# Performance work log

Measured on AMD Instinct MI355X. Metric: run time of the kernel, lower is better.

Reference implementation:

```python
import jax, jax.numpy as jnp
import numpy as np
import math

NHEADS = 8


def pos_encoding_2d(d_model, H, W):
    dm = d_model // 2
    div = jnp.exp(jnp.arange(0, dm, 2, dtype=jnp.float32) * (-math.log(10000.0) / dm))  # [dm//2]
    pw = jnp.arange(W, dtype=jnp.float32)[:, None] * div  # [W, dm//2]
    ph = jnp.arange(H, dtype=jnp.float32)[:, None] * div  # [H, dm//2]
    pe = jnp.zeros((d_model, H, W), jnp.float32)
    pe = pe.at[0:dm:2].set(jnp.broadcast_to(jnp.sin(pw).T[:, None, :], (dm // 2, H, W)))
    pe = pe.at[1:dm:2].set(jnp.broadcast_to(jnp.cos(pw).T[:, None, :], (dm // 2, H, W)))
    pe = pe.at[dm::2].set(jnp.broadcast_to(jnp.sin(ph).T[:, :, None], (dm // 2, H, W)))
    pe = pe.at[dm + 1::2].set(jnp.broadcast_to(jnp.cos(ph).T[:, :, None], (dm // 2, H, W)))
    return pe


def conv_same(x, w, b):
    y = jax.lax.conv_general_dilated(x, w, (1, 1), 'SAME',
                                     dimension_numbers=('NCHW', 'OIHW', 'NCHW'))
    return y + b[None, :, None, None]


def layernorm(x, g, b, eps=1e-5):
    mu = x.mean(-1, keepdims=True)
    var = ((x - mu) ** 2).mean(-1, keepdims=True)
    return (x - mu) / jnp.sqrt(var + eps) * g + b


def setup_inputs() -> dict:
    key = jax.random.key(0)
    B, C, H, W = 8, 256, 32, 32
    KQV, NH, K = 64, NHEADS, 3
    ks = jax.random.split(key, 16)
    s_conv = 1.0 / math.sqrt(C * K * K)
    s_lin = 1.0 / math.sqrt(NH * KQV)
    s_ff = 1.0 / math.sqrt(C)
    return {
        'x': jax.random.normal(ks[0], (B, C, H, W), jnp.float32),
        'Wk': jax.random.normal(ks[1], (NH * KQV, C, K, K), jnp.float32) * s_conv,
        'bk': jax.random.normal(ks[2], (NH * KQV,), jnp.float32) * s_conv,
        'Wq': jax.random.normal(ks[3], (NH * KQV, C, K, K), jnp.float32) * s_conv,
        'bq': jax.random.normal(ks[4], (NH * KQV,), jnp.float32) * s_conv,
        'Wv': jax.random.normal(ks[5], (NH * KQV, C, K, K), jnp.float32) * s_conv,
        'bv': jax.random.normal(ks[6], (NH * KQV,), jnp.float32) * s_conv,
        'Wproj': jax.random.normal(ks[7], (C, NH * KQV), jnp.float32) * s_lin,
        'bproj': jax.random.normal(ks[8], (C,), jnp.float32) * s_lin,
        'ln_g': jnp.ones((C,), jnp.float32),
        'ln_b': jnp.zeros((C,), jnp.float32),
        'W1': jax.random.normal(ks[9], (C, C), jnp.float32) * s_ff,
        'b1': jax.random.normal(ks[10], (C,), jnp.float32) * s_ff,
        'W2': jax.random.normal(ks[11], (C, C), jnp.float32) * s_ff,
        'b2': jax.random.normal(ks[12], (C,), jnp.float32) * s_ff,
    }


def reference(x, Wk, bk, Wq, bq, Wv, bv, Wproj, bproj, ln_g, ln_b, W1, b1, W2, b2):
    B, C, H, W = x.shape
    N = H * W
    pe = pos_encoding_2d(C, H, W)
    xp = x + pe[None]                                   # [B,C,H,W]
    xflat = xp.reshape(B, C, N).transpose(0, 2, 1)      # [B,N,C]

    def heads(w, b):
        return conv_same(xp, w, b).reshape(B, NHEADS, -1, N)  # [B,h,c,N]

    k = heads(Wk, bk)
    q = heads(Wq, bq)
    v = heads(Wv, bv)
    scores = jnp.einsum('bhcn,bhcm->bhnm', k, q) / N    # K^T Q / N, [B,h,N,N]
    sm = jax.nn.softmax(scores, axis=1)                 # Softmax2d -> over HEAD dim (faithful)
    att = jnp.einsum('bhnm,bhcm->bhnc', sm, v)          # [B,h,N,c]
    att = att.transpose(0, 2, 3, 1).reshape(B, N, -1)   # [B,N,c*h] (channel-major, head-minor)
    attproj = att @ Wproj.T + bproj                     # [B,N,C]
    addnormed = layernorm(xflat + attproj, ln_g, ln_b)
    h1 = addnormed @ W1.T + b1
    h1 = jnp.where(h1 > 0, h1, 0.1 * h1)                # LeakyReLU(0.1)
    h2 = h1 @ W2.T + b2
    out = layernorm(h2 + addnormed, ln_g, ln_b)         # same LN params reused (faithful)
    return out.transpose(0, 2, 1).reshape(B, C, H, W)
```

## Files before the change

### kernel.cpp

```cpp
#include <hip/hip_runtime.h>
#include <stdint.h>

typedef __attribute__((ext_vector_type(8))) short short8;
typedef __attribute__((ext_vector_type(4))) short s16x4;
typedef __attribute__((ext_vector_type(4))) float f32x4;

#define DEVI __device__ __forceinline__

#if __has_builtin(__builtin_amdgcn_mfma_f32_16x16x16_bf16)
#define MFMA16(a, b, c) __builtin_amdgcn_mfma_f32_16x16x16_bf16(a, b, c, 0, 0, 0)
#else
#define MFMA16(a, b, c) __builtin_amdgcn_mfma_f32_16x16x16bf16_1k(a, b, c, 0, 0, 0)
#endif

DEVI unsigned short f2bf(float f) {
  union { float f; uint32_t u; } v; v.f = f;
  return (unsigned short)((v.u + 0x7fffu + ((v.u >> 16) & 1u)) >> 16);
}

DEVI float bf2f(uint32_t hi16) {
  union { uint32_t u; float f; } v; v.u = hi16;
  return v.f;
}

DEVI uint32_t pkbf(float a, float b) {
  union { float f; uint32_t u; } x, y; x.f = a; y.f = b;
  return ((x.u + 0x8000u) >> 16) | (((y.u + 0x8000u) >> 16) << 16);
}

DEVI void gload_lds16(const void* g, void* l) {
  __builtin_amdgcn_global_load_lds(
      (const __attribute__((address_space(1))) uint32_t*)g,
      (__attribute__((address_space(3))) uint32_t*)l, 16, 0, 0);
}

__global__ void k_petab(float* __restrict__ T, float* __restrict__ zp) {
  int c = threadIdx.x;
  zp[c] = 0.0f;
  int idx = ((c >= 128) ? c - 128 : c) >> 1;
  float freq = expf(-(float)idx * (logf(10000.0f) / 64.0f));
  for (int p = 0; p < 32; ++p) {
    float ang = (float)p * freq;
    T[c * 32 + p] = (c & 1) ? cosf(ang) : sinf(ang);
  }
}

__global__ __launch_bounds__(256) void k_xpt(const float* __restrict__ x,
                                             const float* __restrict__ T,
                                             unsigned short* __restrict__ xpt_bf,
                                             float* __restrict__ xpt_f) {
  __shared__ __align__(16) float tile[32][36];
  const int b = blockIdx.z, c0 = blockIdx.x * 32, n0 = blockIdx.y * 32;
  const int t = threadIdx.x;
  {
    const int cl = t >> 3, ng = (t & 7) * 4;
    const int c = c0 + cl;
    float4 v = *(const float4*)(x + ((size_t)b * 256 + c) * 1024 + n0 + ng);
    float p0, p1, p2, p3;
    if (c < 128) {
      p0 = T[c * 32 + ng + 0]; p1 = T[c * 32 + ng + 1];
      p2 = T[c * 32 + ng + 2]; p3 = T[c * 32 + ng + 3];
    } else {
      p0 = p1 = p2 = p3 = T[c * 32 + (n0 >> 5)];
    }
    tile[ng + 0][cl] = v.x + p0;
    tile[ng + 1][cl] = v.y + p1;
    tile[ng + 2][cl] = v.z + p2;
    tile[ng + 3][cl] = v.w + p3;
  }
  __syncthreads();
  {
    const int nl = t >> 3, cg = (t & 7) * 4;
    float o0 = tile[nl][cg + 0], o1 = tile[nl][cg + 1];
    float o2 = tile[nl][cg + 2], o3 = tile[nl][cg + 3];
    size_t row = (size_t)b * 1024 + n0 + nl;
    *(float4*)(xpt_f + row * 256 + c0 + cg) = make_float4(o0, o1, o2, o3);
    uint32_t lo = (uint32_t)f2bf(o0) | ((uint32_t)f2bf(o1) << 16);
    uint32_t hi = (uint32_t)f2bf(o2) | ((uint32_t)f2bf(o3) << 16);
    *(uint2*)(xpt_bf + row * 256 + c0 + cg) = make_uint2(lo, hi);
  }
}

__global__ void k_packall(const float* __restrict__ Wk, const float* __restrict__ Wq,
                          const float* __restrict__ Wv, const float* __restrict__ bk,
                          const float* __restrict__ bq, const float* __restrict__ bv,
                          const float* __restrict__ Wproj, const float* __restrict__ W1,
                          const float* __restrict__ W2, unsigned short* __restrict__ Wpack,
                          float* __restrict__ bias_kqv, unsigned short* __restrict__ WprojP,
                          unsigned short* __restrict__ W1b, unsigned short* __restrict__ W2b) {
  int bid = blockIdx.x;
  if (bid < 13824) {
    int i = bid * 256 + threadIdx.x;
    if (i >= 1536 * 2304) return;
    int o = i / 2304, kn = i % 2304;
    int ci = kn & 255, khw = kn >> 8;
    const float* src = (o < 512) ? Wk : ((o < 1024) ? Wq : Wv);
    int oo = o & 511;
    Wpack[i] = f2bf(src[((size_t)oo * 256 + ci) * 9 + khw]);
  } else {
    int i = (bid - 13824) * 256 + threadIdx.x;
    if (i < 1536)
      bias_kqv[i] = (i < 512) ? bk[i] : ((i < 1024) ? bq[i - 512] : bv[i - 1024]);
    {
      int j = i >> 9, f = i & 511;
      int h = f >> 6, c = f & 63;
      unsigned short v = f2bf(Wproj[(size_t)j * 512 + c * 8 + h]);
      WprojP[(size_t)j * 1024 + f] = v;
      WprojP[(size_t)j * 1024 + 512 + f] = v;
    }
    if (i < 65536) {
      W1b[i] = f2bf(W1[i]);
      W2b[i] = f2bf(W2[i]);
    }
  }
}

__global__ __launch_bounds__(256, 2) void k_gemm_conv(const unsigned short* __restrict__ xpt,
                                                      const unsigned short* __restrict__ Wp,
                                                      unsigned short* __restrict__ kqv,
                                                      const float* __restrict__ bias,
                                                      const char* __restrict__ zp) {
  __shared__ __align__(16) unsigned short As[2][128 * 64];
  __shared__ __align__(16) unsigned short Bs[2][128 * 64];
  const int tid = threadIdx.x, l = tid & 63, w = tid >> 6;
  const int wm = w >> 1, wn = w & 1, g = l >> 4, ln = l & 15;
  const int m0 = blockIdx.x * 128, n0 = blockIdx.y * 128;
  const int swz = (l & 7) ^ (l >> 3);

  int rA[4];
  const char* pAbase[4];
  const char* pA[4];
#pragma unroll
  for (int j = 0; j < 4; ++j) {
    int r = m0 + (w * 4 + j) * 8 + (l >> 3);
    rA[j] = r;
    pAbase[j] = (const char*)xpt + ((size_t)r * 256 + swz * 8) * 2;
  }
  const char* pB[4];
#pragma unroll
  for (int j = 0; j < 4; ++j) {
    int r = n0 + (w * 4 + j) * 8 + (l >> 3);
    pB[j] = (const char*)Wp + ((size_t)r * 2304 + swz * 8) * 2;
  }

  f32x4 acc[4][4] = {};

  auto setA = [&](int khw) {
    int d3 = (khw * 11) >> 5;
    int dy = d3 - 1, dx = khw - d3 * 3 - 1;
    int off = (dy * 32 + dx) * 512;
#pragma unroll
    for (int j = 0; j < 4; ++j) {
      int y = ((rA[j] >> 5) & 31) + dy;
      int x = (rA[j] & 31) + dx;
      pA[j] = (((unsigned)y < 32u) && ((unsigned)x < 32u)) ? (pAbase[j] + off) : zp;
    }
  };
  auto STAGE = [&](int buf) {
#pragma unroll
    for (int j = 0; j < 4; ++j) {
      gload_lds16(pA[j], (char*)As + buf * 16384 + (w * 4 + j) * 1024);
      pA[j] += 128;
    }
#pragma unroll
    for (int j = 0; j < 4; ++j) {
      gload_lds16(pB[j], (char*)Bs + buf * 16384 + (w * 4 + j) * 1024);
      pB[j] += 128;
    }
  };
  auto COMPUTE = [&](int buf) {
    const char* Ab2 = (const char*)As + buf * 16384;
    const char* Bb2 = (const char*)Bs + buf * 16384;
#pragma unroll
    for (int kk = 0; kk < 2; ++kk) {
      short8 af[4], bfr[4];
#pragma unroll
      for (int fm = 0; fm < 4; ++fm)
        af[fm] = *(const short8*)(Ab2 + (wm * 64 + fm * 16 + ln) * 128 +
                                  (((kk * 4 + g) ^ (ln & 7)) * 16));
#pragma unroll
      for (int fn = 0; fn < 4; ++fn)
        bfr[fn] = *(const short8*)(Bb2 + (wn * 64 + fn * 16 + ln) * 128 +
                                   (((kk * 4 + g) ^ (ln & 7)) * 16));
#pragma unroll
      for (int fm = 0; fm < 4; ++fm)
#pragma unroll
        for (int fn = 0; fn < 4; ++fn)
          acc[fm][fn] = __builtin_amdgcn_mfma_f32_16x16x32_bf16(af[fm], bfr[fn], acc[fm][fn], 0, 0, 0);
    }
  };

  setA(0);
  STAGE(0);
#pragma unroll
  for (int s = 0; s < 36; ++s) {
    const int buf = s & 1;
    if (s < 35) {
      if (((s + 1) & 3) == 0) setA((s + 1) >> 2);
      STAGE(buf ^ 1);
      asm volatile("s_waitcnt vmcnt(8)" ::: "memory");
    } else {
      asm volatile("s_waitcnt vmcnt(0)" ::: "memory");
    }
    __builtin_amdgcn_s_barrier();
    __builtin_amdgcn_sched_barrier(0);
    COMPUTE(buf);
    asm volatile("s_waitcnt lgkmcnt(0)" ::: "memory");
    __builtin_amdgcn_s_barrier();
    __builtin_amdgcn_sched_barrier(0);
  }

#pragma unroll
  for (int fm = 0; fm < 4; ++fm)
#pragma unroll
    for (int fn = 0; fn < 4; ++fn) {
      int col = n0 + wn * 64 + fn * 16 + ln;
      float bb = bias[col];
#pragma unroll
      for (int r = 0; r < 4; ++r) {
        int row = m0 + wm * 64 + fm * 16 + g * 4 + r;
        kqv[(size_t)row * 1536 + col] = f2bf(acc[fm][fn][r] + bb);
      }
    }
}

template <int EPI, bool ASPLIT>
__global__ __launch_bounds__(256) void k_gemm64(const unsigned short* __restrict__ A,
                                                const unsigned short* __restrict__ B,
                                                void* __restrict__ Cout,
                                                const float* __restrict__ bias,
                                                const float* __restrict__ resid,
                                                int N, int K) {
  __shared__ __align__(16) unsigned short As[128 * 64];
  __shared__ __align__(16) unsigned short Bs[64 * 64];
  const int tid = threadIdx.x, l = tid & 63, w = tid >> 6;
  const int g = l >> 4, ln = l & 15;
  const int m0 = blockIdx.x * 128, n0 = blockIdx.y * 64;
  const int swz = (l & 7) ^ (l >> 3);
  f32x4 acc[2][4] = {};

  for (int kt = 0; kt < K; kt += 64) {
#pragma unroll
    for (int j = 0; j < 4; ++j) {
      int seg = w * 4 + j;
      int r8 = seg * 8 + (l >> 3);
      const char* src;
      if (ASPLIT)
        src = (const char*)A + (((size_t)(kt >> 9) * 8192 * 512) +
                                (size_t)(m0 + r8) * 512 + (kt & 511) + swz * 8) * 2;
      else
        src = (const char*)A + ((size_t)(m0 + r8) * K + kt + swz * 8) * 2;
      gload_lds16(src, (char*)As + seg * 1024);
    }
#pragma unroll
    for (int j = 0; j < 2; ++j) {
      int seg = w * 2 + j;
      int r8 = seg * 8 + (l >> 3);
      gload_lds16((const char*)B + ((size_t)(n0 + r8) * K + kt + swz * 8) * 2,
                  (char*)Bs + seg * 1024);
    }
    __syncthreads();
#pragma unroll
    for (int kk = 0; kk < 2; ++kk) {
      short8 af[2], bfr[4];
#pragma unroll
      for (int fm = 0; fm < 2; ++fm)
        af[fm] = *(const short8*)((const char*)As + (w * 32 + fm * 16 + ln) * 128 +
                                  (((kk * 4 + g) ^ (ln & 7)) * 16));
#pragma unroll
      for (int fn = 0; fn < 4; ++fn)
        bfr[fn] = *(const short8*)((const char*)Bs + (fn * 16 + ln) * 128 +
                                   (((kk * 4 + g) ^ (ln & 7)) * 16));
#pragma unroll
      for (int fm = 0; fm < 2; ++fm)
#pragma unroll
        for (int fn = 0; fn < 4; ++fn)
          acc[fm][fn] = __builtin_amdgcn_mfma_f32_16x16x32_bf16(af[fm], bfr[fn], acc[fm][fn], 0, 0, 0);
    }
    __syncthreads();
  }

#pragma unroll
  for (int fm = 0; fm < 2; ++fm)
#pragma unroll
    for (int fn = 0; fn < 4; ++fn)
#pragma unroll
      for (int r = 0; r < 4; ++r) {
        int row = m0 + w * 32 + fm * 16 + g * 4 + r;
        int col = n0 + fn * 16 + ln;
        float v = acc[fm][fn][r] + bias[col];
        size_t cidx = (size_t)row * N + col;
        if (EPI == 2) {
          ((float*)Cout)[cidx] = v + resid[cidx];
        } else {
          v = (v > 0.f) ? v : 0.1f * v;
          ((unsigned short*)Cout)[cidx] = f2bf(v);
        }
      }
}

__global__ __launch_bounds__(512, 4) void k_attn(const unsigned short* __restrict__ kqv,
                                                 unsigned short* __restrict__ part) {
  __shared__ __align__(16) unsigned short Qs[16][512];
  __shared__ __align__(16) unsigned short Vlin[16][512];
  __shared__ __align__(16) unsigned short Vs[32][16][16];
  __shared__ __align__(16) float sums[4][2][64][4];
  const int tid = threadIdx.x, l = tid & 63, w = tid >> 6;
  const int g = l >> 4, ln = l & 15;
  const int nt = w & 1, hg = w >> 1;
  const int id = blockIdx.x;
  const int b = id & 7, ng = (id >> 3) & 31, ch = id >> 8;
  const int n0 = ng * 32 + nt * 16;
  const int m_base = ch * 512;
  const size_t rowBase = (size_t)b * 1024;
  const float SC = 1.0f / 1024.0f;

  short8 ak[2][2];
#pragma unroll
  for (int hl = 0; hl < 2; ++hl)
#pragma unroll
    for (int kk = 0; kk < 2; ++kk)
      ak[hl][kk] = *(const short8*)&kqv[(rowBase + n0 + ln) * 1536 +
                                        (hg * 2 + hl) * 64 + kk * 32 + g * 8];

  f32x4 acc[2][4] = {};

  auto STAGE = [&](int m0s) {
#pragma unroll
    for (int i = 0; i < 2; ++i) {
      int row = w * 2 + i;
      const unsigned short* src = kqv + (rowBase + m0s + row) * 1536;
      gload_lds16(src + 512 + ((l ^ (row & 7)) * 8), (char*)Qs + row * 1024);
      gload_lds16(src + 1024 + ((l ^ (row & 7)) * 8), (char*)Vlin + row * 1024);
    }
  };

  STAGE(m_base);
  asm volatile("s_waitcnt vmcnt(0)" ::: "memory");
  __builtin_amdgcn_s_barrier();
  __builtin_amdgcn_sched_barrier(0);

  const uint32_t vsBase = (uint32_t)(uintptr_t)&Vs[0][0][0] + l * 8;

  for (int s = 0; s < 32; ++s) {
    {
      const int tm = l & 15;
#pragma unroll
      for (int i = 0; i < 2; ++i) {
        int tch = (l >> 4) + w * 4 + i * 32;
        short8 tv = *(const short8*)((const char*)Vlin + tm * 1024 +
                                     ((tch ^ (tm & 7)) * 16));
        *(short8*)((char*)Vs + (tch >> 1) * 512 + tm * 32 + (tch & 1) * 16) = tv;
      }
    }

    f32x4 sv[2] = {};
#pragma unroll
    for (int kk = 0; kk < 2; ++kk)
#pragma unroll
      for (int hl = 0; hl < 2; ++hl) {
        int chq = (hg * 2 + hl) * 8 + kk * 4 + g;
        short8 qa = *(const short8*)((const char*)Qs + ln * 1024 +
                                     ((chq ^ (ln & 7)) * 16));
        sv[hl] = __builtin_amdgcn_mfma_f32_16x16x32_bf16(qa, ak[hl][kk], sv[hl], 0, 0, 0);
      }

    f32x4 e0, e1, ps;
#pragma unroll
    for (int j = 0; j < 4; ++j) {
      e0[j] = __expf(sv[0][j] * SC);
      e1[j] = __expf(sv[1][j] * SC);
      ps[j] = e0[j] + e1[j];
    }
    *(f32x4*)&sums[hg][nt][l][0] = ps;
    asm volatile("s_waitcnt lgkmcnt(0)" ::: "memory");
    __builtin_amdgcn_s_barrier();
    __builtin_amdgcn_sched_barrier(0);

    if (s < 31) STAGE(m_base + (s + 1) * 16);

    f32x4 tot = ps;
#pragma unroll
    for (int d = 1; d < 4; ++d) {
      f32x4 o = *(const f32x4*)&sums[(hg + d) & 3][nt][l][0];
      tot[0] += o[0]; tot[1] += o[1]; tot[2] += o[2]; tot[3] += o[3];
    }
    f32x4 inv;
#pragma unroll
    for (int j = 0; j < 4; ++j) inv[j] = 1.0f / tot[j];

    s16x4 vf[8];
#pragma unroll
    for (int hl = 0; hl < 2; ++hl) {
      uint32_t ah = vsBase + (hg * 2 + hl) * 2048;
      asm volatile("ds_read_b64_tr_b16 %0, %1" : "=v"(vf[hl * 4 + 0]) : "v"(ah));
      asm volatile("ds_read_b64_tr_b16 %0, %1 offset:512" : "=v"(vf[hl * 4 + 1]) : "v"(ah));
      asm volatile("ds_read_b64_tr_b16 %0, %1 offset:1024" : "=v"(vf[hl * 4 + 2]) : "v"(ah));
      asm volatile("ds_read_b64_tr_b16 %0, %1 offset:1536" : "=v"(vf[hl * 4 + 3]) : "v"(ah));
    }
    asm volatile("s_waitcnt lgkmcnt(0)" ::: "memory");
    __builtin_amdgcn_sched_barrier(0);
    union { uint32_t u[2]; s16x4 v4; } pc0, pc1;
    pc0.u[0] = pkbf(e0[0] * inv[0], e0[1] * inv[1]);
    pc0.u[1] = pkbf(e0[2] * inv[2], e0[3] * inv[3]);
    pc1.u[0] = pkbf(e1[0] * inv[0], e1[1] * inv[1]);
    pc1.u[1] = pkbf(e1[2] * inv[2], e1[3] * inv[3]);
#pragma unroll
    for (int cf = 0; cf < 4; ++cf) {
      acc[0][cf] = MFMA16(vf[cf], pc0.v4, acc[0][cf]);
      acc[1][cf] = MFMA16(vf[4 + cf], pc1.v4, acc[1][cf]);
    }

    asm volatile("s_waitcnt vmcnt(0)" ::: "memory");
    __builtin_amdgcn_s_barrier();
    __builtin_amdgcn_sched_barrier(0);
  }

  const size_t outBase = (size_t)ch * 8192 * 512 + (rowBase + n0 + ln) * 512;
#pragma unroll
  for (int hl = 0; hl < 2; ++hl)
#pragma unroll
    for (int cf = 0; cf < 4; ++cf)
#pragma unroll
      for (int r2 = 0; r2 < 2; ++r2) {
        int c = (hg * 2 + hl) * 64 + cf * 16 + g * 4 + r2 * 2;
        uint32_t u = (uint32_t)f2bf(acc[hl][cf][2 * r2]) |
                     ((uint32_t)f2bf(acc[hl][cf][2 * r2 + 1]) << 16);
        *(uint32_t*)&part[outBase + c] = u;
      }
}

__global__ __launch_bounds__(256) void k_ln0(const float* __restrict__ in,
                                             const float* __restrict__ g,
                                             const float* __restrict__ bta,
                                             float* __restrict__ out_f,
                                             unsigned short* __restrict__ out_b) {
  const int l = threadIdx.x & 63, w = threadIdx.x >> 6;
  const size_t row = (size_t)blockIdx.x * 4 + w;
  float4 xv = *(const float4*)(in + row * 256 + l * 4);
  float s = xv.x + xv.y + xv.z + xv.w;
  float q = xv.x * xv.x + xv.y * xv.y + xv.z * xv.z + xv.w * xv.w;
#pragma unroll
  for (int o = 1; o < 64; o <<= 1) {
    s += __shfl_xor(s, o, 64);
    q += __shfl_xor(q, o, 64);
  }
  float mu = s * (1.0f / 256.0f);
  float var = q * (1.0f / 256.0f) - mu * mu;
  float rstd = rsqrtf(var + 1e-5f);
  float4 gv = *(const float4*)(g + l * 4);
  float4 bv = *(const float4*)(bta + l * 4);
  float o0 = (xv.x - mu) * rstd * gv.x + bv.x;
  float o1 = (xv.y - mu) * rstd * gv.y + bv.y;
  float o2 = (xv.z - mu) * rstd * gv.z + bv.z;
  float o3 = (xv.w - mu) * rstd * gv.w + bv.w;
  *(float4*)(out_f + row * 256 + l * 4) = make_float4(o0, o1, o2, o3);
  uint32_t lo = (uint32_t)f2bf(o0) | ((uint32_t)f2bf(o1) << 16);
  uint32_t hi = (uint32_t)f2bf(o2) | ((uint32_t)f2bf(o3) << 16);
  *(uint2*)(out_b + row * 256 + l * 4) = make_uint2(lo, hi);
}

__global__ __launch_bounds__(256) void k_ffn2out(const unsigned short* __restrict__ h1,
                                                 const unsigned short* __restrict__ W2b,
                                                 const float* __restrict__ b2,
                                                 const float* __restrict__ addnf,
                                                 const float* __restrict__ lg,
                                                 const float* __restrict__ lb,
                                                 float* __restrict__ out) {
  __shared__ __align__(16) unsigned short As[32 * 64];
  __shared__ __align__(16) unsigned short Bs[256 * 64];
  __shared__ __align__(16) float Tt[256][33];
  __shared__ float rsum[4][32][2];
  const int tid = threadIdx.x, l = tid & 63, w = tid >> 6;
  const int g4 = l >> 4, ln = l & 15;
  const int m0 = blockIdx.x * 32;
  const int swz = (l & 7) ^ (l >> 3);
  f32x4 acc[2][4] = {};

  for (int kt = 0; kt < 256; kt += 64) {
    gload_lds16((const char*)h1 + ((size_t)(m0 + w * 8 + (l >> 3)) * 256 + kt + swz * 8) * 2,
                (char*)As + w * 1024);
#pragma unroll
    for (int j = 0; j < 8; ++j) {
      int seg = w * 8 + j;
      gload_lds16((const char*)W2b + ((size_t)(seg * 8 + (l >> 3)) * 256 + kt + swz * 8) * 2,
                  (char*)Bs + seg * 1024);
    }
    __syncthreads();
#pragma unroll
    for (int kk = 0; kk < 2; ++kk) {
      short8 af[2], bfr[4];
#pragma unroll
      for (int fm = 0; fm < 2; ++fm)
        af[fm] = *(const short8*)((const char*)As + (fm * 16 + ln) * 128 +
                                  (((kk * 4 + g4) ^ (ln & 7)) * 16));
#pragma unroll
      for (int fn = 0; fn < 4; ++fn)
        bfr[fn] = *(const short8*)((const char*)Bs + (w * 64 + fn * 16 + ln) * 128 +
                                   (((kk * 4 + g4) ^ (ln & 7)) * 16));
#pragma unroll
      for (int fm = 0; fm < 2; ++fm)
#pragma unroll
        for (int fn = 0; fn < 4; ++fn)
          acc[fm][fn] = __builtin_amdgcn_mfma_f32_16x16x32_bf16(af[fm], bfr[fn], acc[fm][fn], 0, 0, 0);
    }
    __syncthreads();
  }

  float vals[2][4][4];
#pragma unroll
  for (int fm = 0; fm < 2; ++fm)
#pragma unroll
    for (int r = 0; r < 4; ++r) {
      int row_l = fm * 16 + g4 * 4 + r;
      float s = 0.f, q = 0.f;
#pragma unroll
      for (int fn = 0; fn < 4; ++fn) {
        int col = w * 64 + fn * 16 + ln;
        float v = acc[fm][fn][r] + b2[col] + addnf[(size_t)(m0 + row_l) * 256 + col];
        vals[fm][fn][r] = v;
        s += v;
        q += v * v;
      }
#pragma unroll
      for (int o = 1; o < 16; o <<= 1) {
        s += __shfl_xor(s, o, 64);
        q += __shfl_xor(q, o, 64);
      }
      if (ln == 0) {
        rsum[w][row_l][0] = s;
        rsum[w][row_l][1] = q;
      }
    }
  __syncthreads();

#pragma unroll
  for (int fm = 0; fm < 2; ++fm)
#pragma unroll
    for (int r = 0; r < 4; ++r) {
      int row_l = fm * 16 + g4 * 4 + r;
      float s = rsum[0][row_l][0] + rsum[1][row_l][0] + rsum[2][row_l][0] + rsum[3][row_l][0];
      float q = rsum[0][row_l][1] + rsum[1][row_l][1] + rsum[2][row_l][1] + rsum[3][row_l][1];
      float mu = s * (1.0f / 256.0f);
      float rstd = rsqrtf(q * (1.0f / 256.0f) - mu * mu + 1e-5f);
#pragma unroll
      for (int fn = 0; fn < 4; ++fn) {
        int col = w * 64 + fn * 16 + ln;
        Tt[col][row_l] = (vals[fm][fn][r] - mu) * rstd * lg[col] + lb[col];
      }
    }
  __syncthreads();

  const int bimg = m0 >> 10, nn0 = m0 & 1023;
#pragma unroll
  for (int i = 0; i < 8; ++i) {
    int c = i * 32 + (tid >> 3);
    int ng = (tid & 7) * 4;
    float4 o = make_float4(Tt[c][ng], Tt[c][ng + 1], Tt[c][ng + 2], Tt[c][ng + 3]);
    *(float4*)&out[((size_t)bimg * 256 + c) * 1024 + nn0 + ng] = o;
  }
}

extern "C" void kernel_launch(void* const* d_in, const int* in_sizes, int n_in,
                              void* d_out, int out_size, void* d_ws, size_t ws_size,
                              hipStream_t stream) {
  const float* x     = (const float*)d_in[0];
  const float* Wk    = (const float*)d_in[1];
  const float* bk    = (const float*)d_in[2];
  const float* Wq    = (const float*)d_in[3];
  const float* bq    = (const float*)d_in[4];
  const float* Wv    = (const float*)d_in[5];
  const float* bv    = (const float*)d_in[6];
  const float* Wproj = (const float*)d_in[7];
  const float* bproj = (const float*)d_in[8];
  const float* ln_g  = (const float*)d_in[9];
  const float* ln_b  = (const float*)d_in[10];
  const float* W1    = (const float*)d_in[11];
  const float* b1    = (const float*)d_in[12];
  const float* W2    = (const float*)d_in[13];
  const float* b2    = (const float*)d_in[14];

  char* ws = (char*)d_ws;
  constexpr size_t OFF_XPTB  = 0;
  constexpr size_t OFF_XPTF  = OFF_XPTB  + (size_t)8192 * 256 * 2;
  constexpr size_t OFF_WPACK = OFF_XPTF  + (size_t)8192 * 256 * 4;
  constexpr size_t OFF_BIAS  = OFF_WPACK + (size_t)1536 * 2304 * 2;
  constexpr size_t OFF_WPROJ = OFF_BIAS  + (size_t)1536 * 4;
  constexpr size_t OFF_W1B   = OFF_WPROJ + (size_t)256 * 1024 * 2;
  constexpr size_t OFF_W2B   = OFF_W1B   + (size_t)256 * 256 * 2;
  constexpr size_t OFF_PET   = OFF_W2B   + (size_t)256 * 256 * 2;
  constexpr size_t OFF_ZERO  = OFF_PET   + (size_t)256 * 32 * 4;
  constexpr size_t OFF_KQV   = OFF_ZERO  + 1024;
  constexpr size_t OFF_PART  = OFF_KQV   + (size_t)8192 * 1536 * 2;
  constexpr size_t OFF_Y1    = OFF_PART  + (size_t)2 * 8192 * 512 * 2;
  constexpr size_t OFF_ADDNF = OFF_Y1    + (size_t)8192 * 256 * 4;
  constexpr size_t OFF_ADDNB = OFF_ADDNF + (size_t)8192 * 256 * 4;
  constexpr size_t OFF_H1    = OFF_ADDNB + (size_t)8192 * 256 * 2;

  (void)in_sizes; (void)n_in; (void)out_size; (void)ws_size;

  const char* zp = (const char*)(ws + OFF_ZERO);

  k_petab<<<1, 256, 0, stream>>>((float*)(ws + OFF_PET), (float*)(ws + OFF_ZERO));
  k_xpt<<<dim3(8, 32, 8), 256, 0, stream>>>(x, (const float*)(ws + OFF_PET),
                                            (unsigned short*)(ws + OFF_XPTB),
                                            (float*)(ws + OFF_XPTF));
  k_packall<<<14336, 256, 0, stream>>>(Wk, Wq, Wv, bk, bq, bv, Wproj, W1, W2,
                                       (unsigned short*)(ws + OFF_WPACK),
                                       (float*)(ws + OFF_BIAS),
                                       (unsigned short*)(ws + OFF_WPROJ),
                                       (unsigned short*)(ws + OFF_W1B),
                                       (unsigned short*)(ws + OFF_W2B));
  k_gemm_conv<<<dim3(64, 12), 256, 0, stream>>>(
      (const unsigned short*)(ws + OFF_XPTB), (const unsigned short*)(ws + OFF_WPACK),
      (unsigned short*)(ws + OFF_KQV), (const float*)(ws + OFF_BIAS), zp);
  k_attn<<<dim3(512), 512, 0, stream>>>((const unsigned short*)(ws + OFF_KQV),
                                        (unsigned short*)(ws + OFF_PART));
  k_gemm64<2, true><<<dim3(64, 4), 256, 0, stream>>>(
      (const unsigned short*)(ws + OFF_PART), (const unsigned short*)(ws + OFF_WPROJ),
      ws + OFF_Y1, bproj, (const float*)(ws + OFF_XPTF), 256, 1024);
  k_ln0<<<2048, 256, 0, stream>>>((const float*)(ws + OFF_Y1), ln_g, ln_b,
                                  (float*)(ws + OFF_ADDNF), (unsigned short*)(ws + OFF_ADDNB));
  k_gemm64<3, false><<<dim3(64, 4), 256, 0, stream>>>(
      (const unsigned short*)(ws + OFF_ADDNB), (const unsigned short*)(ws + OFF_W1B),
      ws + OFF_H1, b1, nullptr, 256, 256);
  k_ffn2out<<<256, 256, 0, stream>>>((const unsigned short*)(ws + OFF_H1),
                                     (const unsigned short*)(ws + OFF_W2B), b2,
                                     (const float*)(ws + OFF_ADDNF), ln_g, ln_b,
                                     (float*)d_out);
}
```

Before: 206.2 us.

## Widen conv GEMM tile to 192 columns and fuse projection with layernorm

Changes the conv implicit-GEMM tile from 128x128 to 128x192, so the grid shrinks from 64x12 to 64x8 blocks and each wave does 4x6 MFMAs per k-step. This raises operand reuse and cuts redundant A loads, at the cost of more registers and LDS. The attention-output projection GEMM is merged with the residual add and first layernorm into one kernel that computes full 256-column rows per block. That removes the intermediate fp32 Y1 buffer round-trip and one launch, but the fused kernel runs only 256 blocks.

After: 192.8 us. 1.07x faster.

```diff
diff --git a/kernel.cpp b/kernel.cpp
--- a/kernel.cpp
+++ b/kernel.cpp
@@ -121,84 +121,86 @@
                                                       const float* __restrict__ bias,
                                                       const char* __restrict__ zp) {
   __shared__ __align__(16) unsigned short As[2][128 * 64];
-  __shared__ __align__(16) unsigned short Bs[2][128 * 64];
+  __shared__ __align__(16) unsigned short Bs[2][192 * 64];
   const int tid = threadIdx.x, l = tid & 63, w = tid >> 6;
   const int wm = w >> 1, wn = w & 1, g = l >> 4, ln = l & 15;
-  const int m0 = blockIdx.x * 128, n0 = blockIdx.y * 128;
+  const int m0 = blockIdx.x * 128, n0 = blockIdx.y * 192;
   const int swz = (l & 7) ^ (l >> 3);
 
-  int rA[4];
   const char* pAbase[4];
-  const char* pA[4];
 #pragma unroll
   for (int j = 0; j < 4; ++j) {
     int r = m0 + (w * 4 + j) * 8 + (l >> 3);
-    rA[j] = r;
     pAbase[j] = (const char*)xpt + ((size_t)r * 256 + swz * 8) * 2;
   }
-  const char* pB[4];
-#pragma unroll
-  for (int j = 0; j < 4; ++j) {
-    int r = n0 + (w * 4 + j) * 8 + (l >> 3);
-    pB[j] = (const char*)Wp + ((size_t)r * 2304 + swz * 8) * 2;
-  }
-
-  f32x4 acc[4][4] = {};
-
-  auto setA = [&](int khw) {
-    int d3 = (khw * 11) >> 5;
-    int dy = d3 - 1, dx = khw - d3 * 3 - 1;
-    int off = (dy * 32 + dx) * 512;
+  const char* pB0 = (const char*)Wp +
+                    ((size_t)(n0 + w * 48 + (l >> 3)) * 2304 + swz * 8) * 2;
+
+  f32x4 acc[4][6] = {};
+  int vmask = 0;
+  int aoff = 0;
+
+  auto setTap = [&](int tap) {
+    int d3 = (tap * 11) >> 5;
+    int dy = d3 - 1, dx = tap - d3 * 3 - 1;
+    aoff = (dy * 32 + dx) * 512;
+    int m = 0;
 #pragma unroll
     for (int j = 0; j < 4; ++j) {
-      int y = ((rA[j] >> 5) & 31) + dy;
-      int x = (rA[j] & 31) + dx;
-      pA[j] = (((unsigned)y < 32u) && ((unsigned)x < 32u)) ? (pAbase[j] + off) : zp;
-    }
+      int r = m0 + (w * 4 + j) * 8 + (l >> 3);
+      int y = ((r >> 5) & 31) + dy;
+      int x = (r & 31) + dx;
+      if (((unsigned)y < 32u) && ((unsigned)x < 32u)) m |= (1 << j);
+    }
+    vmask = m;
   };
-  auto STAGE = [&](int buf) {
+
+  auto STAGE = [&](int buf, int kb) {
 #pragma unroll
     for (int j = 0; j < 4; ++j) {
-      gload_lds16(pA[j], (char*)As + buf * 16384 + (w * 4 + j) * 1024);
-      pA[j] += 128;
-    }
-#pragma unroll
-    for (int j = 0; j < 4; ++j) {
-      gload_lds16(pB[j], (char*)Bs + buf * 16384 + (w * 4 + j) * 1024);
-      pB[j] += 128;
+      const char* a = (vmask & (1 << j)) ? (pAbase[j] + aoff) : zp;
+      gload_lds16(a, (char*)As + buf * 16384 + (w * 4 + j) * 1024);
+    }
+#pragma unroll
+    for (int j = 0; j < 6; ++j) {
+      gload_lds16(pB0 + j * 36864 + kb, (char*)Bs + buf * 24576 + (w * 6 + j) * 1024);
     }
   };
+
   auto COMPUTE = [&](int buf) {
     const char* Ab2 = (const char*)As + buf * 16384;
-    const char* Bb2 = (const char*)Bs + buf * 16384;
+    const char* Bb2 = (const char*)Bs + buf * 24576;
 #pragma unroll
     for (int kk = 0; kk < 2; ++kk) {
-      short8 af[4], bfr[4];
+      short8 af[4], bfr[6];
 #pragma unroll
       for (int fm = 0; fm < 4; ++fm)
         af[fm] = *(const short8*)(Ab2 + (wm * 64 + fm * 16 + ln) * 128 +
                                   (((kk * 4 + g) ^ (ln & 7)) * 16));
 #pragma unroll
-      for (int fn = 0; fn < 4; ++fn)
-        bfr[fn] = *(const short8*)(Bb2 + (wn * 64 + fn * 16 + ln) * 128 +
+      for (int fn = 0; fn < 6; ++fn)
+        bfr[fn] = *(const short8*)(Bb2 + (wn * 96 + fn * 16 + ln) * 128 +
                                    (((kk * 4 + g) ^ (ln & 7)) * 16));
 #pragma unroll
       for (int fm = 0; fm < 4; ++fm)
 #pragma unroll
-        for (int fn = 0; fn < 4; ++fn)
+        for (int fn = 0; fn < 6; ++fn)
           acc[fm][fn] = __builtin_amdgcn_mfma_f32_16x16x32_bf16(af[fm], bfr[fn], acc[fm][fn], 0, 0, 0);
     }
   };
 
-  setA(0);
-  STAGE(0);
-#pragma unroll
+  setTap(0);
+  STAGE(0, 0);
+  aoff += 128;
+  int kb = 128;
   for (int s = 0; s < 36; ++s) {
     const int buf = s & 1;
     if (s < 35) {
-      if (((s + 1) & 3) == 0) setA((s + 1) >> 2);
-      STAGE(buf ^ 1);
-      asm volatile("s_waitcnt vmcnt(8)" ::: "memory");
+      if (((s + 1) & 3) == 0) setTap((s + 1) >> 2);
+      STAGE(buf ^ 1, kb);
+      kb += 128;
+      aoff += 128;
+      asm volatile("s_waitcnt vmcnt(10)" ::: "memory");
     } else {
       asm volatile("s_waitcnt vmcnt(0)" ::: "memory");
     }
@@ -213,8 +215,8 @@
 #pragma unroll
   for (int fm = 0; fm < 4; ++fm)
 #pragma unroll
-    for (int fn = 0; fn < 4; ++fn) {
-      int col = n0 + wn * 64 + fn * 16 + ln;
+    for (int fn = 0; fn < 6; ++fn) {
+      int col = n0 + wn * 96 + fn * 16 + ln;
       float bb = bias[col];
 #pragma unroll
       for (int r = 0; r < 4; ++r) {
@@ -224,13 +226,10 @@
     }
 }
 
-template <int EPI, bool ASPLIT>
-__global__ __launch_bounds__(256) void k_gemm64(const unsigned short* __restrict__ A,
-                                                const unsigned short* __restrict__ B,
-                                                void* __restrict__ Cout,
-                                                const float* __restrict__ bias,
-                                                const float* __restrict__ resid,
-                                                int N, int K) {
+__global__ __launch_bounds__(256) void k_ffn1(const unsigned short* __restrict__ A,
+                                              const unsigned short* __restrict__ B,
+                                              unsigned short* __restrict__ Cout,
+                                              const float* __restrict__ bias) {
   __shared__ __align__(16) unsigned short As[128 * 64];
   __shared__ __align__(16) unsigned short Bs[64 * 64];
   const int tid = threadIdx.x, l = tid & 63, w = tid >> 6;
@@ -239,24 +238,19 @@
   const int swz = (l & 7) ^ (l >> 3);
   f32x4 acc[2][4] = {};
 
-  for (int kt = 0; kt < K; kt += 64) {
+  for (int kt = 0; kt < 256; kt += 64) {
 #pragma unroll
     for (int j = 0; j < 4; ++j) {
       int seg = w * 4 + j;
       int r8 = seg * 8 + (l >> 3);
-      const char* src;
-      if (ASPLIT)
-        src = (const char*)A + (((size_t)(kt >> 9) * 8192 * 512) +
-                                (size_t)(m0 + r8) * 512 + (kt & 511) + swz * 8) * 2;
-      else
-        src = (const char*)A + ((size_t)(m0 + r8) * K + kt + swz * 8) * 2;
-      gload_lds16(src, (char*)As + seg * 1024);
+      gload_lds16((const char*)A + ((size_t)(m0 + r8) * 256 + kt + swz * 8) * 2,
+                  (char*)As + seg * 1024);
     }
 #pragma unroll
     for (int j = 0; j < 2; ++j) {
       int seg = w * 2 + j;
       int r8 = seg * 8 + (l >> 3);
-      gload_lds16((const char*)B + ((size_t)(n0 + r8) * K + kt + swz * 8) * 2,
+      gload_lds16((const char*)B + ((size_t)(n0 + r8) * 256 + kt + swz * 8) * 2,
                   (char*)Bs + seg * 1024);
     }
     __syncthreads();
@@ -289,13 +283,8 @@
         int row = m0 + w * 32 + fm * 16 + g * 4 + r;
         int col = n0 + fn * 16 + ln;
         float v = acc[fm][fn][r] + bias[col];
-        size_t cidx = (size_t)row * N + col;
-        if (EPI == 2) {
-          ((float*)Cout)[cidx] = v + resid[cidx];
-        } else {
-          v = (v > 0.f) ? v : 0.1f * v;
-          ((unsigned short*)Cout)[cidx] = f2bf(v);
-        }
+        v = (v > 0.f) ? v : 0.1f * v;
+        Cout[(size_t)row * 256 + col] = f2bf(v);
       }
 }
 
@@ -430,34 +419,100 @@
       }
 }
 
-__global__ __launch_bounds__(256) void k_ln0(const float* __restrict__ in,
-                                             const float* __restrict__ g,
-                                             const float* __restrict__ bta,
-                                             float* __restrict__ out_f,
-                                             unsigned short* __restrict__ out_b) {
-  const int l = threadIdx.x & 63, w = threadIdx.x >> 6;
-  const size_t row = (size_t)blockIdx.x * 4 + w;
-  float4 xv = *(const float4*)(in + row * 256 + l * 4);
-  float s = xv.x + xv.y + xv.z + xv.w;
-  float q = xv.x * xv.x + xv.y * xv.y + xv.z * xv.z + xv.w * xv.w;
-#pragma unroll
-  for (int o = 1; o < 64; o <<= 1) {
-    s += __shfl_xor(s, o, 64);
-    q += __shfl_xor(q, o, 64);
-  }
-  float mu = s * (1.0f / 256.0f);
-  float var = q * (1.0f / 256.0f) - mu * mu;
-  float rstd = rsqrtf(var + 1e-5f);
-  float4 gv = *(const float4*)(g + l * 4);
-  float4 bv = *(const float4*)(bta + l * 4);
-  float o0 = (xv.x - mu) * rstd * gv.x + bv.x;
-  float o1 = (xv.y - mu) * rstd * gv.y + bv.y;
-  float o2 = (xv.z - mu) * rstd * gv.z + bv.z;
-  float o3 = (xv.w - mu) * rstd * gv.w + bv.w;
-  *(float4*)(out_f + row * 256 + l * 4) = make_float4(o0, o1, o2, o3);
-  uint32_t lo = (uint32_t)f2bf(o0) | ((uint32_t)f2bf(o1) << 16);
-  uint32_t hi = (uint32_t)f2bf(o2) | ((uint32_t)f2bf(o3) << 16);
-  *(uint2*)(out_b + row * 256 + l * 4) = make_uint2(lo, hi);
+__global__ __launch_bounds__(256) void k_projln(const unsigned short* __restrict__ part,
+                                                const unsigned short* __restrict__ Wp,
+                                                const float* __restrict__ bias,
+                                                const float* __restrict__ resid,
+                                                const float* __restrict__ lg,
+                                                const float* __restrict__ lb,
+                                                float* __restrict__ out_f,
+                                                unsigned short* __restrict__ out_b) {
+  __shared__ __align__(16) unsigned short As[32 * 64];
+  __shared__ __align__(16) unsigned short Bs[256 * 64];
+  __shared__ float rsum[4][32][2];
+  const int tid = threadIdx.x, l = tid & 63, w = tid >> 6;
+  const int g4 = l >> 4, ln = l & 15;
+  const int m0 = blockIdx.x * 32;
+  const int swz = (l & 7) ^ (l >> 3);
+  f32x4 acc[2][4] = {};
+
+  for (int kt = 0; kt < 1024; kt += 64) {
+    gload_lds16((const char*)part + (((size_t)(kt >> 9) * 8192 * 512) +
+                                     (size_t)(m0 + w * 8 + (l >> 3)) * 512 +
+                                     (kt & 511) + swz * 8) * 2,
+                (char*)As + w * 1024);
+#pragma unroll
+    for (int j = 0; j < 8; ++j) {
+      int seg = w * 8 + j;
+      gload_lds16((const char*)Wp + ((size_t)(seg * 8 + (l >> 3)) * 1024 + kt + swz * 8) * 2,
+                  (char*)Bs + seg * 1024);
+    }
+    __syncthreads();
+#pragma unroll
+    for (int kk = 0; kk < 2; ++kk) {
+      short8 af[2], bfr[4];
+#pragma unroll
+      for (int fm = 0; fm < 2; ++fm)
+        af[fm] = *(const short8*)((const char*)As + (fm * 16 + ln) * 128 +
+                                  (((kk * 4 + g4) ^ (ln & 7)) * 16));
+#pragma unroll
+      for (int fn = 0; fn < 4; ++fn)
+        bfr[fn] = *(const short8*)((const char*)Bs + (w * 64 + fn * 16 + ln) * 128 +
+                                   (((kk * 4 + g4) ^ (ln & 7)) * 16));
+#pragma unroll
+      for (int fm = 0; fm < 2; ++fm)
+#pragma unroll
+        for (int fn = 0; fn < 4; ++fn)
+          acc[fm][fn] = __builtin_amdgcn_mfma_f32_16x16x32_bf16(af[fm], bfr[fn], acc[fm][fn], 0, 0, 0);
+    }
+    __syncthreads();
+  }
+
+  float vals[2][4][4];
+#pragma unroll
+  for (int fm = 0; fm < 2; ++fm)
+#pragma unroll
+    for (int r = 0; r < 4; ++r) {
+      int row_l = fm * 16 + g4 * 4 + r;
+      float s = 0.f, q = 0.f;
+#pragma unroll
+      for (int fn = 0; fn < 4; ++fn) {
+        int col = w * 64 + fn * 16 + ln;
+        float v = acc[fm][fn][r] + bias[col] + resid[(size_t)(m0 + row_l) * 256 + col];
+        vals[fm][fn][r] = v;
+        s += v;
+        q += v * v;
+      }
+#pragma unroll
+      for (int o = 1; o < 16; o <<= 1) {
+        s += __shfl_xor(s, o, 64);
+        q += __shfl_xor(q, o, 64);
+      }
+      if (ln == 0) {
+        rsum[w][row_l][0] = s;
+        rsum[w][row_l][1] = q;
+      }
+    }
+  __syncthreads();
+
+#pragma unroll
+  for (int fm = 0; fm < 2; ++fm)
+#pragma unroll
+    for (int r = 0; r < 4; ++r) {
+      int row_l = fm * 16 + g4 * 4 + r;
+      float s = rsum[0][row_l][0] + rsum[1][row_l][0] + rsum[2][row_l][0] + rsum[3][row_l][0];
+      float q = rsum[0][row_l][1] + rsum[1][row_l][1] + rsum[2][row_l][1] + rsum[3][row_l][1];
+      float mu = s * (1.0f / 256.0f);
+      float rstd = rsqrtf(q * (1.0f / 256.0f) - mu * mu + 1e-5f);
+      size_t rowOff = (size_t)(m0 + row_l) * 256;
+#pragma unroll
+      for (int fn = 0; fn < 4; ++fn) {
+        int col = w * 64 + fn * 16 + ln;
+        float o = (vals[fm][fn][r] - mu) * rstd * lg[col] + lb[col];
+        out_f[rowOff + col] = o;
+        out_b[rowOff + col] = f2bf(o);
+      }
+    }
 }
 
 __global__ __launch_bounds__(256) void k_ffn2out(const unsigned short* __restrict__ h1,
@@ -592,8 +647,7 @@
   constexpr size_t OFF_ZERO  = OFF_PET   + (size_t)256 * 32 * 4;
   constexpr size_t OFF_KQV   = OFF_ZERO  + 1024;
   constexpr size_t OFF_PART  = OFF_KQV   + (size_t)8192 * 1536 * 2;
-  constexpr size_t OFF_Y1    = OFF_PART  + (size_t)2 * 8192 * 512 * 2;
-  constexpr size_t OFF_ADDNF = OFF_Y1    + (size_t)8192 * 256 * 4;
+  constexpr size_t OFF_ADDNF = OFF_PART  + (size_t)2 * 8192 * 512 * 2;
   constexpr size_t OFF_ADDNB = OFF_ADDNF + (size_t)8192 * 256 * 4;
   constexpr size_t OFF_H1    = OFF_ADDNB + (size_t)8192 * 256 * 2;
 
@@ -611,19 +665,18 @@
                                        (unsigned short*)(ws + OFF_WPROJ),
                                        (unsigned short*)(ws + OFF_W1B),
                                        (unsigned short*)(ws + OFF_W2B));
-  k_gemm_conv<<<dim3(64, 12), 256, 0, stream>>>(
+  k_gemm_conv<<<dim3(64, 8), 256, 0, stream>>>(
       (const unsigned short*)(ws + OFF_XPTB), (const unsigned short*)(ws + OFF_WPACK),
       (unsigned short*)(ws + OFF_KQV), (const float*)(ws + OFF_BIAS), zp);
   k_attn<<<dim3(512), 512, 0, stream>>>((const unsigned short*)(ws + OFF_KQV),
                                         (unsigned short*)(ws + OFF_PART));
-  k_gemm64<2, true><<<dim3(64, 4), 256, 0, stream>>>(
-      (const unsigned short*)(ws + OFF_PART), (const unsigned short*)(ws + OFF_WPROJ),
-      ws + OFF_Y1, bproj, (const float*)(ws + OFF_XPTF), 256, 1024);
-  k_ln0<<<2048, 256, 0, stream>>>((const float*)(ws + OFF_Y1), ln_g, ln_b,
-                                  (float*)(ws + OFF_ADDNF), (unsigned short*)(ws + OFF_ADDNB));
-  k_gemm64<3, false><<<dim3(64, 4), 256, 0, stream>>>(
+  k_projln<<<256, 256, 0, stream>>>((const unsigned short*)(ws + OFF_PART),
+                                    (const unsigned short*)(ws + OFF_WPROJ), bproj,
+                                    (const float*)(ws + OFF_XPTF), ln_g, ln_b,
+                                    (float*)(ws + OFF_ADDNF), (unsigned short*)(ws + OFF_ADDNB));
+  k_ffn1<<<dim3(64, 4), 256, 0, stream>>>(
       (const unsigned short*)(ws + OFF_ADDNB), (const unsigned short*)(ws + OFF_W1B),
-      ws + OFF_H1, b1, nullptr, 256, 256);
+      (unsigned short*)(ws + OFF_H1), b1);
   k_ffn2out<<<256, 256, 0, stream>>>((const unsigned short*)(ws + OFF_H1),
                                      (const unsigned short*)(ws + OFF_W2B), b2,
                                      (const float*)(ws + OFF_ADDNF), ln_g, ln_b,
```
